# Optimization experiments

Hardware: AMD Instinct MI355X
Metric: run time of the kernel (lower is better)

The kernel has to match this reference:

```python
import jax, jax.numpy as jnp
import numpy as np

N_NODES = 50000
N_EDGES = 600000
N_GRAPHS = 256
D = 128          # hidden_dim
L = 4            # num_layer
OUT = 1          # output_dim
ATOM_DIMS = [119, 5, 12, 12, 10, 6, 6, 2, 2]   # table size = dim+1, pad to 120
BOND_DIMS = [6, 6, 2, 2, 2]                    # table size = dim+1, pad to 7
BN_EPS = 1e-5


def setup_inputs() -> dict:
    key = jax.random.key(0)
    ks = jax.random.split(key, 16)
    x = jax.random.randint(ks[0], (N_NODES, 9), 0, 3)
    edge_index = jax.random.randint(ks[1], (2, N_EDGES), 0, N_NODES)
    edge_attr = jax.random.randint(ks[2], (N_EDGES, 5), 0, 3)
    batch = jnp.sort(jax.random.randint(ks[3], (N_NODES,), 0, N_GRAPHS))
    s = 0.1
    # padded atom embedding tables: [9, 120, D] (rows beyond dim+1 unused)
    atom_emb = jax.random.normal(ks[4], (9, 120, D), jnp.float32) * s
    # padded bond tables per layer: [L, 5, 7, D]
    bond_emb = jax.random.normal(ks[5], (L, 5, 7, D), jnp.float32) * s
    lin_w = jax.random.normal(ks[6], (L, D, D), jnp.float32) * (1.0 / np.sqrt(D))
    lin_b = jnp.zeros((L, D), jnp.float32)
    bn_gamma = jnp.ones((L, D), jnp.float32)
    bn_beta = jnp.zeros((L, D), jnp.float32)
    mlp_w1 = jax.random.normal(ks[7], (D // 2, D), jnp.float32) * (1.0 / np.sqrt(D))
    mlp_b1 = jnp.zeros((D // 2,), jnp.float32)
    mlp_w2 = jax.random.normal(ks[8], (OUT, D // 2), jnp.float32) * (1.0 / np.sqrt(D // 2))
    mlp_b2 = jnp.zeros((OUT,), jnp.float32)
    return dict(x=x, edge_index=edge_index, edge_attr=edge_attr, batch=batch,
                atom_emb=atom_emb, bond_emb=bond_emb, lin_w=lin_w, lin_b=lin_b,
                bn_gamma=bn_gamma, bn_beta=bn_beta,
                mlp_w1=mlp_w1, mlp_b1=mlp_b1, mlp_w2=mlp_w2, mlp_b2=mlp_b2)


def _multi_embed(tables, idx):
    # tables: [F, V, D], idx: [N, F] -> sum_f tables[f][idx[:, f]]
    return jax.vmap(lambda t, i: t[i], in_axes=(0, 1))(tables, idx).sum(0)


def reference(x, edge_index, edge_attr, batch, atom_emb, bond_emb, lin_w, lin_b,
              bn_gamma, bn_beta, mlp_w1, mlp_b1, mlp_w2, mlp_b2):
    n = x.shape[0]
    loop = jnp.arange(n, dtype=edge_index.dtype)
    src = jnp.concatenate([edge_index[0], loop])           # x_j (source)
    dst = jnp.concatenate([edge_index[1], loop])           # aggregate into target i
    ea = jnp.concatenate([edge_attr, jnp.zeros((n, 5), edge_attr.dtype)], axis=0)
    h = _multi_embed(atom_emb, x)                          # [N, D]
    for l in range(L):
        e_emb = _multi_embed(bond_emb[l], ea)              # [E+N, D]
        msg = h[src] + e_emb                               # gather + add
        aggr = jax.ops.segment_sum(msg, dst, num_segments=n)
        z = aggr @ lin_w[l].T + lin_b[l]
        mu = z.mean(0)
        var = z.var(0)                                     # biased, matches torch BN fwd
        h = jax.nn.relu((z - mu) * jax.lax.rsqrt(var + BN_EPS) * bn_gamma[l] + bn_beta[l])
    # global mean pool
    sums = jax.ops.segment_sum(h, batch, num_segments=N_GRAPHS)
    cnt = jax.ops.segment_sum(jnp.ones((n,), h.dtype), batch, num_segments=N_GRAPHS)
    g = sums / jnp.maximum(cnt, 1.0)[:, None]
    # MLP head (dropout inactive at inference)
    out = jax.nn.relu(g @ mlp_w1.T + mlp_b1) @ mlp_w2.T + mlp_b2
    return out
```

## Files before the change

### kernel.cpp

```cpp
#include <hip/hip_runtime.h>
#include <hip/hip_bf16.h>
#include <stdint.h>

#define D 128
#define NGRAPH 256
#define BN_EPS 1e-5f
#define NCOMBO 243
#define AGG_BLOCKS 256
#define AGG_THREADS 1024
#define MAXDEG 48
#define GEMM_ROWS 128

typedef unsigned short u16;
typedef __attribute__((ext_vector_type(8))) short bf16x8;
typedef __attribute__((ext_vector_type(4))) float f32x4;

__device__ inline u16 f2bf(float a) {
  return __builtin_bit_cast(u16, __float2bfloat16(a));
}
__device__ inline uint32_t pk2(float a, float b) {
  return (uint32_t)f2bf(a) | ((uint32_t)f2bf(b) << 16);
}
__device__ inline float bflo(uint32_t u) { return __builtin_bit_cast(float, u << 16); }
__device__ inline float bfhi(uint32_t u) { return __builtin_bit_cast(float, u & 0xffff0000u); }
__device__ inline void unpack8(uint4 v, float* f) {
  f[0] = bflo(v.x); f[1] = bfhi(v.x); f[2] = bflo(v.y); f[3] = bfhi(v.y);
  f[4] = bflo(v.z); f[5] = bfhi(v.z); f[6] = bflo(v.w); f[7] = bfhi(v.w);
}

__global__ __launch_bounds__(256) void setup_kernel(
    const int* __restrict__ x, const float* __restrict__ atom_emb,
    float* __restrict__ h0,
    const int* __restrict__ src, const int* __restrict__ dst,
    const int* __restrict__ attr, int* __restrict__ deg,
    uint2* __restrict__ edges, int ne,
    const int* __restrict__ batch, int* __restrict__ goff,
    float* __restrict__ gsum, int n) {
  int b = blockIdx.x, tid = threadIdx.x;
  int nscat = (ne + 255) >> 8;
  int nemb = (n * 32 + 255) >> 8;
  if (b < nscat) {
    int e = b * 256 + tid;
    if (e >= ne) return;
    int d = dst[e];
    int slot = atomicAdd(&deg[d], 1);
    if (slot >= MAXDEG) return;
    int a0 = attr[e * 5 + 0], a1 = attr[e * 5 + 1], a2 = attr[e * 5 + 2];
    int a3 = attr[e * 5 + 3], a4 = attr[e * 5 + 4];
    uint32_t packed = (uint32_t)(a0 * 81 + a1 * 27 + a2 * 9 + a3 * 3 + a4);
    uint2 r; r.x = (uint32_t)src[e]; r.y = packed;
    edges[(size_t)d * MAXDEG + slot] = r;
  } else if (b < nscat + nemb) {
    int t = (b - nscat) * 256 + tid;
    int node = t >> 5, cq = t & 31;
    if (node >= n) return;
    float4 acc = {0.f, 0.f, 0.f, 0.f};
#pragma unroll
    for (int f = 0; f < 9; f++) {
      int idx = x[node * 9 + f];
      const float4* row = (const float4*)(atom_emb + ((size_t)f * 120 + idx) * D);
      float4 v = row[cq];
      acc.x += v.x; acc.y += v.y; acc.z += v.z; acc.w += v.w;
    }
    ((float4*)(h0 + (size_t)node * D))[cq] = acc;
  } else {
    if (b == nscat + nemb) {
      for (int t = tid; t < 4 * 2 * D; t += 256) gsum[t] = 0.f;
    }
    int i = (b - nscat - nemb) * 256 + tid;
    if (i >= n) return;
    int bb = batch[i];
    if (i == 0) {
      for (int g = 0; g <= bb; g++) goff[g] = 0;
    } else {
      int pb = batch[i - 1];
      for (int g = pb + 1; g <= bb; g++) goff[g] = i;
    }
    if (i == n - 1) {
      for (int g = bb + 1; g <= NGRAPH; g++) goff[g] = n;
    }
  }
}

__global__ __launch_bounds__(128) void prep_kernel(
    const float* __restrict__ bemb, const float* __restrict__ linw,
    float* __restrict__ tabC, u16* __restrict__ wball) {
  __shared__ float row[D];
  int b = blockIdx.x, c = threadIdx.x;
  if (b < 4 * NCOMBO) {
    int l = b / NCOMBO, r = b % NCOMBO;
    const float* bond = bemb + (size_t)l * 5 * 7 * D;
    const float* W = linw + (size_t)l * D * D;
    int a0 = r / 81, a1 = (r / 27) % 3, a2 = (r / 9) % 3, a3 = (r / 3) % 3,
        a4 = r % 3;
    float v = bond[(0 * 7 + a0) * D + c] + bond[(1 * 7 + a1) * D + c] +
              bond[(2 * 7 + a2) * D + c] + bond[(3 * 7 + a3) * D + c] +
              bond[(4 * 7 + a4) * D + c];
    row[c] = v;
    __syncthreads();
    float s = 0.f;
    for (int k = 0; k < D; k++) s += row[k] * W[(size_t)c * D + k];
    tabC[((size_t)l * NCOMBO + r) * D + c] = s;
  } else {
    int i = b - 4 * NCOMBO;
    int l = i >> 7, j = i & 127;
    float v = linw[(size_t)l * D * D + (size_t)j * D + c];
    wball[(size_t)l * D * D + (size_t)j * D + (c ^ ((j & 7) << 3))] = f2bf(v);
  }
}

__global__ __launch_bounds__(256) void gemm_kernel(const float* __restrict__ in,
                                                   const u16* __restrict__ Wb,
                                                   const float* __restrict__ gsum,
                                                   const float* __restrict__ gamma,
                                                   const float* __restrict__ beta,
                                                   float invN,
                                                   u16* __restrict__ out, int M) {
  __shared__ u16 wlds[D * D];
  __shared__ float bns[2 * D];
  int tid = threadIdx.x;
  for (int i = tid; i < D * D / 8; i += 256)
    ((uint4*)wlds)[i] = ((const uint4*)Wb)[i];
  if (gsum && tid < D) {
    float s = gsum[tid], q = gsum[D + tid];
    float mu = s * invN;
    float var = q * invN - mu * mu;
    float sc = rsqrtf(var + BN_EPS) * gamma[tid];
    bns[tid] = sc;
    bns[D + tid] = beta[tid] - mu * sc;
  }
  __syncthreads();

  int wave = tid >> 6, lane = tid & 63;
  int quad = lane >> 4, l16 = lane & 15;
  int m0 = blockIdx.x * GEMM_ROWS + wave * 32;

  f32x4 acc[2][8];
#pragma unroll
  for (int mt = 0; mt < 2; mt++)
#pragma unroll
    for (int t = 0; t < 8; t++) acc[mt][t] = (f32x4){0.f, 0.f, 0.f, 0.f};

#pragma unroll
  for (int kk = 0; kk < 4; kk++) {
    int k0 = kk * 32 + quad * 8;
    bf16x8 a[2];
#pragma unroll
    for (int mt = 0; mt < 2; mt++) {
      int m = m0 + mt * 16 + l16;
      if (m < M) {
        float4 v0 = *(const float4*)(in + (size_t)m * D + k0);
        float4 v1 = *(const float4*)(in + (size_t)m * D + k0 + 4);
        if (gsum) {
          float4 sc0 = *(const float4*)(bns + k0);
          float4 sc1 = *(const float4*)(bns + k0 + 4);
          float4 sh0 = *(const float4*)(bns + D + k0);
          float4 sh1 = *(const float4*)(bns + D + k0 + 4);
          v0.x = fmaxf(v0.x * sc0.x + sh0.x, 0.f);
          v0.y = fmaxf(v0.y * sc0.y + sh0.y, 0.f);
          v0.z = fmaxf(v0.z * sc0.z + sh0.z, 0.f);
          v0.w = fmaxf(v0.w * sc0.w + sh0.w, 0.f);
          v1.x = fmaxf(v1.x * sc1.x + sh1.x, 0.f);
          v1.y = fmaxf(v1.y * sc1.y + sh1.y, 0.f);
          v1.z = fmaxf(v1.z * sc1.z + sh1.z, 0.f);
          v1.w = fmaxf(v1.w * sc1.w + sh1.w, 0.f);
        }
        uint4 pa = {pk2(v0.x, v0.y), pk2(v0.z, v0.w), pk2(v1.x, v1.y), pk2(v1.z, v1.w)};
        a[mt] = __builtin_bit_cast(bf16x8, pa);
      } else {
        uint4 pz = {0u, 0u, 0u, 0u};
        a[mt] = __builtin_bit_cast(bf16x8, pz);
      }
    }
#pragma unroll
    for (int nt = 0; nt < 8; nt++) {
      int nrow = nt * 16 + l16;
      uint4 braw = *(const uint4*)(wlds + nrow * D + (k0 ^ ((nrow & 7) << 3)));
      bf16x8 bfrag = __builtin_bit_cast(bf16x8, braw);
      acc[0][nt] = __builtin_amdgcn_mfma_f32_16x16x32_bf16(a[0], bfrag, acc[0][nt], 0, 0, 0);
      acc[1][nt] = __builtin_amdgcn_mfma_f32_16x16x32_bf16(a[1], bfrag, acc[1][nt], 0, 0, 0);
    }
  }
#pragma unroll
  for (int mt = 0; mt < 2; mt++)
#pragma unroll
    for (int r = 0; r < 4; r++) {
      int row = m0 + mt * 16 + quad * 4 + r;
      if (row < M) {
#pragma unroll
        for (int nt = 0; nt < 8; nt++)
          out[(size_t)row * D + nt * 16 + l16] = f2bf(acc[mt][nt][r]);
      }
    }
}

__global__ __launch_bounds__(AGG_THREADS) void agg_kernel(
    const u16* __restrict__ ht, const float* __restrict__ tabC,
    const float* __restrict__ linb, const uint2* __restrict__ edges,
    const int* __restrict__ deg, float* __restrict__ z,
    float* __restrict__ gsum, int n) {
  __shared__ float tabs[NCOMBO * D];
  __shared__ float psum[2 * D];
  int tid = threadIdx.x;
  for (int i = tid; i < NCOMBO * D / 4; i += AGG_THREADS)
    ((float4*)tabs)[i] = ((const float4*)tabC)[i];
  if (tid < 2 * D) psum[tid] = 0.f;
  __syncthreads();

  int lane = tid & 63;
  int g = lane >> 4;
  int c8 = lane & 15;
  int wid = (blockIdx.x * AGG_THREADS + tid) >> 6;
  int nw = (gridDim.x * AGG_THREADS) >> 6;

  float lbz[8];
  {
    float4 l0 = ((const float4*)linb)[c8 * 2];
    float4 l1 = ((const float4*)linb)[c8 * 2 + 1];
    float4 t0 = *(const float4*)(tabs + c8 * 8);
    float4 t1 = *(const float4*)(tabs + c8 * 8 + 4);
    lbz[0] = l0.x + t0.x; lbz[1] = l0.y + t0.y;
    lbz[2] = l0.z + t0.z; lbz[3] = l0.w + t0.w;
    lbz[4] = l1.x + t1.x; lbz[5] = l1.y + t1.y;
    lbz[6] = l1.z + t1.z; lbz[7] = l1.w + t1.w;
  }
  float ssum[8], ssq[8];
#pragma unroll
  for (int i = 0; i < 8; i++) { ssum[i] = 0.f; ssq[i] = 0.f; }

  int dgv = (wid < n) ? deg[wid] : 0;
  for (int node = wid; node < n; node += nw) {
    int dg = dgv;
    if (node + nw < n) dgv = deg[node + nw];
    int cnt = (dg > MAXDEG) ? MAXDEG : dg;
    int base = node * MAXDEG;
    int e = base + cnt;
    int j = base + g;

    float acc[8];
    if (g == 0) {
      float sv[8];
      unpack8(*(const uint4*)(ht + (size_t)node * D + c8 * 8), sv);
#pragma unroll
      for (int i = 0; i < 8; i++) acc[i] = sv[i] + lbz[i];
    } else {
#pragma unroll
      for (int i = 0; i < 8; i++) acc[i] = 0.f;
    }

    bool v = j < e;
    uint2 rec;
    uint4 hv;
    if (v) rec = edges[j];
    if (v) hv = *(const uint4*)(ht + (size_t)rec.x * D + c8 * 8);
    while (v) {
      int jn = j + 4;
      bool vn = jn < e;
      uint2 recn;
      uint4 hvn;
      if (vn) recn = edges[jn];
      if (vn) hvn = *(const uint4*)(ht + (size_t)recn.x * D + c8 * 8);
      {
        const float* tr = tabs + rec.y * D + c8 * 8;
        float4 b0 = *(const float4*)tr;
        float4 b1 = *(const float4*)(tr + 4);
        float hvf[8];
        unpack8(hv, hvf);
        acc[0] += hvf[0] + b0.x; acc[1] += hvf[1] + b0.y;
        acc[2] += hvf[2] + b0.z; acc[3] += hvf[3] + b0.w;
        acc[4] += hvf[4] + b1.x; acc[5] += hvf[5] + b1.y;
        acc[6] += hvf[6] + b1.z; acc[7] += hvf[7] + b1.w;
      }
      rec = recn; hv = hvn; j = jn; v = vn;
    }

#pragma unroll
    for (int off = 16; off <= 32; off <<= 1)
#pragma unroll
      for (int i = 0; i < 8; i++) acc[i] += __shfl_xor(acc[i], off, 64);
    if (g == 0) {
      float4 za = {acc[0], acc[1], acc[2], acc[3]};
      float4 zb4 = {acc[4], acc[5], acc[6], acc[7]};
      float4* zr = (float4*)(z + (size_t)node * D);
      zr[c8 * 2] = za;
      zr[c8 * 2 + 1] = zb4;
#pragma unroll
      for (int i = 0; i < 8; i++) {
        ssum[i] += acc[i];
        ssq[i] += acc[i] * acc[i];
      }
    }
  }
  if (g == 0) {
    int c0 = c8 * 8;
#pragma unroll
    for (int i = 0; i < 8; i++) {
      atomicAdd(&psum[c0 + i], ssum[i]);
      atomicAdd(&psum[D + c0 + i], ssq[i]);
    }
  }
  __syncthreads();
  if (tid < 2 * D) atomicAdd(&gsum[tid], psum[tid]);
}

__global__ __launch_bounds__(512) void poolmlp_kernel(
    const float* __restrict__ z, const float* __restrict__ gsum,
    const float* __restrict__ gamma, const float* __restrict__ beta,
    float invN, const int* __restrict__ goff,
    const float* __restrict__ w1, const float* __restrict__ b1,
    const float* __restrict__ w2, const float* __restrict__ b2,
    float* __restrict__ out) {
  __shared__ float sdata[512];
  __shared__ float pg[D];
  int g = blockIdx.x;
  int c = threadIdx.x & 127, r4 = threadIdx.x >> 7;
  float s0 = gsum[c], q0 = gsum[D + c];
  float mu = s0 * invN;
  float var = q0 * invN - mu * mu;
  float sc = rsqrtf(var + BN_EPS) * gamma[c];
  float sh = beta[c] - mu * sc;
  int s = goff[g], cnt = goff[g + 1] - s;
  float acc = 0.f;
  for (int i = r4; i < cnt; i += 4) {
    float zv = z[(size_t)(s + i) * D + c];
    acc += fmaxf(zv * sc + sh, 0.f);
  }
  sdata[threadIdx.x] = acc;
  __syncthreads();
  if (r4 == 0) {
    float t = sdata[c] + sdata[128 + c] + sdata[256 + c] + sdata[384 + c];
    pg[c] = t / fmaxf((float)cnt, 1.f);
  }
  __syncthreads();
  if (threadIdx.x < 64) {
    int j = threadIdx.x;
    float v = b1[j];
    for (int k = 0; k < D; k++) v += pg[k] * w1[(size_t)j * D + k];
    v = fmaxf(v, 0.f) * w2[j];
#pragma unroll
    for (int off = 32; off > 0; off >>= 1) v += __shfl_down(v, off, 64);
    if (j == 0) out[g] = v + b2[0];
  }
}

extern "C" void kernel_launch(void* const* d_in, const int* in_sizes, int n_in,
                              void* d_out, int out_size, void* d_ws, size_t ws_size,
                              hipStream_t stream) {
  const int*   x     = (const int*)d_in[0];
  const int*   eidx  = (const int*)d_in[1];
  const int*   eattr = (const int*)d_in[2];
  const int*   batch = (const int*)d_in[3];
  const float* aemb  = (const float*)d_in[4];
  const float* bemb  = (const float*)d_in[5];
  const float* linw  = (const float*)d_in[6];
  const float* linb  = (const float*)d_in[7];
  const float* gamma = (const float*)d_in[8];
  const float* beta  = (const float*)d_in[9];
  const float* w1    = (const float*)d_in[10];
  const float* b1    = (const float*)d_in[11];
  const float* w2    = (const float*)d_in[12];
  const float* b2    = (const float*)d_in[13];
  float* out = (float*)d_out;

  int n  = in_sizes[3];
  int ne = in_sizes[1] / 2;
  float invN = 1.f / (float)n;

  char* p = (char*)d_ws;
  auto alloc = [&](size_t bytes) {
    char* r = p;
    p += (bytes + 255) & ~(size_t)255;
    return r;
  };
  float* bufA   = (float*)alloc((size_t)n * D * 4);
  u16*   bufB   = (u16*)alloc((size_t)n * D * 2);
  uint2* edges  = (uint2*)alloc((size_t)n * MAXDEG * 8);
  int*   deg    = (int*)alloc((size_t)n * 4);
  int*   goff   = (int*)alloc((size_t)(NGRAPH + 1) * 4);
  float* tabC   = (float*)alloc((size_t)4 * NCOMBO * D * 4);
  u16*   wball  = (u16*)alloc((size_t)4 * D * D * 2);
  float* gsum   = (float*)alloc((size_t)4 * 2 * D * 4);

  hipMemsetAsync(deg, 0, (size_t)n * 4, stream);

  int nscat = (ne + 255) >> 8;
  int nemb = (n * 32 + 255) >> 8;
  int ngoff = (n + 255) >> 8;
  setup_kernel<<<nscat + nemb + ngoff, 256, 0, stream>>>(
      x, aemb, bufA, eidx, eidx + ne, eattr, deg, edges, ne, batch, goff,
      gsum, n);
  prep_kernel<<<4 * NCOMBO + 4 * D, 128, 0, stream>>>(bemb, linw, tabC, wball);

  for (int l = 0; l < 4; l++) {
    gemm_kernel<<<(n + GEMM_ROWS - 1) / GEMM_ROWS, 256, 0, stream>>>(
        bufA, wball + (size_t)l * D * D,
        l ? (gsum + (size_t)(l - 1) * 2 * D) : (const float*)nullptr,
        l ? (gamma + (size_t)(l - 1) * D) : (const float*)nullptr,
        l ? (beta + (size_t)(l - 1) * D) : (const float*)nullptr,
        invN, bufB, n);
    agg_kernel<<<AGG_BLOCKS, AGG_THREADS, 0, stream>>>(
        bufB, tabC + (size_t)l * NCOMBO * D, linb + (size_t)l * D, edges, deg,
        bufA, gsum + (size_t)l * 2 * D, n);
  }
  poolmlp_kernel<<<NGRAPH, 512, 0, stream>>>(
      bufA, gsum + 3 * 2 * D, gamma + 3 * D, beta + 3 * D, invN, goff,
      w1, b1, w2, b2, out);
}
```

Before: 405.1 us.

## Drop LDS bond table in aggregation, deepen gather prefetch, raise occupancy

The aggregation kernel no longer stages the 243x128 float combined bond table (about 124 KB) in shared memory. It reads table rows from global memory instead, relying on L1/L2 caching. This frees LDS, so the launch moves to 1280 blocks of 256 threads with a 5-blocks-per-CU bound. The edge loop becomes a deeper software pipeline that loads edge records three steps ahead and features and table rows one to two steps ahead. BN statistics accumulation is split across two lane groups so each holds fewer registers. The cost is global-memory table reads on every edge and more live registers for prefetching.

```diff
diff --git a/kernel.cpp b/kernel.cpp
--- a/kernel.cpp
+++ b/kernel.cpp
@@ -6,8 +6,8 @@
 #define NGRAPH 256
 #define BN_EPS 1e-5f
 #define NCOMBO 243
-#define AGG_BLOCKS 256
-#define AGG_THREADS 1024
+#define AGG_BLOCKS 1280
+#define AGG_THREADS 256
 #define MAXDEG 48
 #define GEMM_ROWS 128
 
@@ -194,16 +194,13 @@
     }
 }
 
-__global__ __launch_bounds__(AGG_THREADS) void agg_kernel(
+__global__ __launch_bounds__(AGG_THREADS, 5) void agg_kernel(
     const u16* __restrict__ ht, const float* __restrict__ tabC,
     const float* __restrict__ linb, const uint2* __restrict__ edges,
     const int* __restrict__ deg, float* __restrict__ z,
     float* __restrict__ gsum, int n) {
-  __shared__ float tabs[NCOMBO * D];
   __shared__ float psum[2 * D];
   int tid = threadIdx.x;
-  for (int i = tid; i < NCOMBO * D / 4; i += AGG_THREADS)
-    ((float4*)tabs)[i] = ((const float4*)tabC)[i];
   if (tid < 2 * D) psum[tid] = 0.f;
   __syncthreads();
 
@@ -217,16 +214,16 @@
   {
     float4 l0 = ((const float4*)linb)[c8 * 2];
     float4 l1 = ((const float4*)linb)[c8 * 2 + 1];
-    float4 t0 = *(const float4*)(tabs + c8 * 8);
-    float4 t1 = *(const float4*)(tabs + c8 * 8 + 4);
+    float4 t0 = *(const float4*)(tabC + c8 * 8);
+    float4 t1 = *(const float4*)(tabC + c8 * 8 + 4);
     lbz[0] = l0.x + t0.x; lbz[1] = l0.y + t0.y;
     lbz[2] = l0.z + t0.z; lbz[3] = l0.w + t0.w;
     lbz[4] = l1.x + t1.x; lbz[5] = l1.y + t1.y;
     lbz[6] = l1.z + t1.z; lbz[7] = l1.w + t1.w;
   }
-  float ssum[8], ssq[8];
-#pragma unroll
-  for (int i = 0; i < 8; i++) { ssum[i] = 0.f; ssq[i] = 0.f; }
+  float st[8];
+#pragma unroll
+  for (int i = 0; i < 8; i++) st[i] = 0.f;
 
   int dgv = (wid < n) ? deg[wid] : 0;
   for (int node = wid; node < n; node += nw) {
@@ -237,10 +234,27 @@
     int e = base + cnt;
     int j = base + g;
 
+    uint4 selfv;
+    if (g == 0) selfv = *(const uint4*)(ht + (size_t)node * D + c8 * 8);
+    bool v0 = j < e, v1 = j + 4 < e, v2 = j + 8 < e;
+    uint2 rA, rY, rX;
+    if (v0) rA = edges[j];
+    if (v1) rY = edges[j + 4];
+    if (v2) rX = edges[j + 8];
+    uint4 hA, hB;
+    float4 tA0, tA1;
+    if (v0) {
+      hA = *(const uint4*)(ht + (size_t)rA.x * D + c8 * 8);
+      const float* tr = tabC + (size_t)rA.y * D + c8 * 8;
+      tA0 = *(const float4*)tr;
+      tA1 = *(const float4*)(tr + 4);
+    }
+    if (v1) hB = *(const uint4*)(ht + (size_t)rY.x * D + c8 * 8);
+
     float acc[8];
     if (g == 0) {
       float sv[8];
-      unpack8(*(const uint4*)(ht + (size_t)node * D + c8 * 8), sv);
+      unpack8(selfv, sv);
 #pragma unroll
       for (int i = 0; i < 8; i++) acc[i] = sv[i] + lbz[i];
     } else {
@@ -248,55 +262,60 @@
       for (int i = 0; i < 8; i++) acc[i] = 0.f;
     }
 
-    bool v = j < e;
-    uint2 rec;
-    uint4 hv;
-    if (v) rec = edges[j];
-    if (v) hv = *(const uint4*)(ht + (size_t)rec.x * D + c8 * 8);
-    while (v) {
-      int jn = j + 4;
-      bool vn = jn < e;
-      uint2 recn;
-      uint4 hvn;
-      if (vn) recn = edges[jn];
-      if (vn) hvn = *(const uint4*)(ht + (size_t)recn.x * D + c8 * 8);
+    while (v0) {
+      bool v3 = j + 12 < e;
+      uint2 rN;
+      if (v3) rN = edges[j + 12];
+      uint4 hC;
+      if (v2) hC = *(const uint4*)(ht + (size_t)rX.x * D + c8 * 8);
+      float4 tB0, tB1;
+      if (v1) {
+        const float* tr = tabC + (size_t)rY.y * D + c8 * 8;
+        tB0 = *(const float4*)tr;
+        tB1 = *(const float4*)(tr + 4);
+      }
       {
-        const float* tr = tabs + rec.y * D + c8 * 8;
-        float4 b0 = *(const float4*)tr;
-        float4 b1 = *(const float4*)(tr + 4);
-        float hvf[8];
-        unpack8(hv, hvf);
-        acc[0] += hvf[0] + b0.x; acc[1] += hvf[1] + b0.y;
-        acc[2] += hvf[2] + b0.z; acc[3] += hvf[3] + b0.w;
-        acc[4] += hvf[4] + b1.x; acc[5] += hvf[5] + b1.y;
-        acc[6] += hvf[6] + b1.z; acc[7] += hvf[7] + b1.w;
+        float hf[8];
+        unpack8(hA, hf);
+        acc[0] += hf[0] + tA0.x; acc[1] += hf[1] + tA0.y;
+        acc[2] += hf[2] + tA0.z; acc[3] += hf[3] + tA0.w;
+        acc[4] += hf[4] + tA1.x; acc[5] += hf[5] + tA1.y;
+        acc[6] += hf[6] + tA1.z; acc[7] += hf[7] + tA1.w;
       }
-      rec = recn; hv = hvn; j = jn; v = vn;
+      hA = hB; hB = hC;
+      tA0 = tB0; tA1 = tB1;
+      rY = rX; rX = rN;
+      v0 = v1; v1 = v2; v2 = v3;
+      j += 4;
     }
 
 #pragma unroll
     for (int off = 16; off <= 32; off <<= 1)
 #pragma unroll
       for (int i = 0; i < 8; i++) acc[i] += __shfl_xor(acc[i], off, 64);
+
     if (g == 0) {
       float4 za = {acc[0], acc[1], acc[2], acc[3]};
       float4 zb4 = {acc[4], acc[5], acc[6], acc[7]};
       float4* zr = (float4*)(z + (size_t)node * D);
       zr[c8 * 2] = za;
       zr[c8 * 2 + 1] = zb4;
-#pragma unroll
-      for (int i = 0; i < 8; i++) {
-        ssum[i] += acc[i];
-        ssq[i] += acc[i] * acc[i];
-      }
-    }
-  }
-  if (g == 0) {
+    } else if (g == 1) {
+#pragma unroll
+      for (int i = 0; i < 8; i++) st[i] += acc[i];
+    } else if (g == 2) {
+#pragma unroll
+      for (int i = 0; i < 8; i++) st[i] += acc[i] * acc[i];
+    }
+  }
+  {
     int c0 = c8 * 8;
-#pragma unroll
-    for (int i = 0; i < 8; i++) {
-      atomicAdd(&psum[c0 + i], ssum[i]);
-      atomicAdd(&psum[D + c0 + i], ssq[i]);
+    if (g == 1) {
+#pragma unroll
+      for (int i = 0; i < 8; i++) atomicAdd(&psum[c0 + i], st[i]);
+    } else if (g == 2) {
+#pragma unroll
+      for (int i = 0; i < 8; i++) atomicAdd(&psum[D + c0 + i], st[i]);
     }
   }
   __syncthreads();
```

Result: slower. 457.4 us (+12.9%).
